# Optimization experiments

Hardware: AMD Instinct MI355X
Metric: run time of the kernel (lower is better)

Reference implementation:

```python
import jax, jax.numpy as jnp
import numpy as np

B, S, LW = 128, 256, 20          # batch, sent len, max word len
VW, VC = 400000, 80              # word / char vocab
DC, DW, HC, HW, NT = 25, 300, 25, 200, 10  # dims from args.dims; NT tags
DIN = DW + 2 * HC                # word-LSTM input dim = 350


def setup_inputs() -> dict:
    key = jax.random.key(0)
    ks = jax.random.split(key, 16)
    s = 0.1
    return {
        "words_batch": jax.random.randint(ks[0], (B, S), 0, VW),
        "chars_batch": jax.random.randint(ks[1], (B, S, LW), 0, VC),
        "lens_word": jnp.sort(jax.random.randint(ks[2], (B,), 1, S + 1))[::-1],
        "emb_char": jax.random.normal(ks[3], (VC + 1, DC), jnp.float32) * s,
        "emb_word": jax.random.normal(ks[4], (VW, DW), jnp.float32) * s,
        "conv_w": jax.random.normal(ks[5], (2 * HC, 1, 3, DC), jnp.float32) * s,
        "conv_b": jnp.zeros((2 * HC,), jnp.float32),
        "w_ih_f": jax.random.normal(ks[6], (4 * HW, DIN), jnp.float32) * s,
        "w_hh_f": jax.random.normal(ks[7], (4 * HW, HW), jnp.float32) * s,
        "b_f": jnp.zeros((4 * HW,), jnp.float32),
        "w_ih_b": jax.random.normal(ks[8], (4 * HW, DIN), jnp.float32) * s,
        "w_hh_b": jax.random.normal(ks[9], (4 * HW, HW), jnp.float32) * s,
        "b_b": jnp.zeros((4 * HW,), jnp.float32),
        "proj_w": jax.random.normal(ks[10], (NT, 2 * HW), jnp.float32) * s,
        "proj_b": jnp.zeros((NT,), jnp.float32),
    }


def _lstm_dir(xg, w_hh, mask, reverse):
    # xg: [S,B,4H] precomputed input-gate contributions; mask: [S,B,1]
    Hh = w_hh.shape[1]
    h0 = jnp.zeros((xg.shape[1], Hh), xg.dtype)
    c0 = jnp.zeros_like(h0)

    def step(carry, inp):
        h, c = carry
        xg_t, m = inp
        g = xg_t + h @ w_hh.T
        i, f, gg, o = jnp.split(g, 4, axis=-1)
        i, f, o = jax.nn.sigmoid(i), jax.nn.sigmoid(f), jax.nn.sigmoid(o)
        gg = jnp.tanh(gg)
        c_new = f * c + i * gg
        h_new = o * jnp.tanh(c_new)
        h = jnp.where(m, h_new, h)
        c = jnp.where(m, c_new, c)
        out = jnp.where(m, h_new, 0.0)  # pad_packed zeros beyond length
        return (h, c), out

    _, out = jax.lax.scan(step, (h0, c0), (xg, mask), reverse=reverse)
    return out  # [S,B,H]


def reference(words_batch, chars_batch, lens_word, emb_char, emb_word,
              conv_w, conv_b, w_ih_f, w_hh_f, b_f, w_ih_b, w_hh_b, b_b,
              proj_w, proj_b):
    # --- char CNN encoder ---
    ec = emb_char[chars_batch]                       # [B,S,LW,DC]
    x = ec.reshape(B * S, 1, LW, DC)
    y = jax.lax.conv_general_dilated(x, conv_w, (1, 1), [(2, 2), (0, 0)])
    y = y + conv_b[None, :, None, None]              # [B*S, 2HC, LW+2, 1]
    out_char = y.max(axis=(2, 3)).reshape(B, S, 2 * HC)
    # --- word features ---
    ew = emb_word[words_batch]                       # [B,S,DW]
    feats = jnp.concatenate([ew, out_char], axis=-1) # [B,S,DIN]
    # --- masked BiLSTM over words (packed-sequence semantics) ---
    mask = (jnp.arange(S)[None, :] < lens_word[:, None])  # [B,S]
    mask_t = mask.T[:, :, None]                      # [S,B,1]
    xf = jnp.einsum('bsd,gd->sbg', feats, w_ih_f) + b_f
    xb = jnp.einsum('bsd,gd->sbg', feats, w_ih_b) + b_b
    hf = _lstm_dir(xf, w_hh_f, mask_t, reverse=False)
    hb = _lstm_dir(xb, w_hh_b, mask_t, reverse=True)
    enc = jnp.concatenate([hf, hb], axis=-1).transpose(1, 0, 2)  # [B,S,2HW]
    # --- emissions ---
    return jnp.einsum('bsh,th->bst', enc, proj_w) + proj_b       # [B,S,NT]
```

## Files before the change

kernel.cpp:

```cpp
#include <hip/hip_runtime.h>

typedef unsigned short u16;
typedef __attribute__((ext_vector_type(4))) unsigned short u16x4;
typedef __attribute__((ext_vector_type(8))) short bf16x8;
typedef __attribute__((ext_vector_type(4))) float f32x4;

#define BB 128
#define SS 256
#define LWW 20
#define NTg 10
#define HWg 200
#define G4 800
#define DWg 300
#define DIN 350
#define KP 352
#define NP 896
#define NW (BB*SS)
#define OUTN (NW*NTg)

__device__ __forceinline__ float b2f(u16 u){ return __uint_as_float(((unsigned)u)<<16); }
__device__ __forceinline__ u16 f2b(float f){
  unsigned x = __float_as_uint(f);
  unsigned r = (x + 0x7fffu + ((x>>16)&1u)) >> 16;
  return (u16)r;
}
__device__ __forceinline__ float ldf(const void* p, long long i, int isb){
  return isb ? b2f(((const u16*)p)[i]) : ((const float*)p)[i];
}
__device__ __forceinline__ int ldi(const void* p, long long i, int i64){
  return i64 ? (int)((const long long*)p)[i] : ((const int*)p)[i];
}
__device__ __forceinline__ f32x4 mfma16(bf16x8 a, bf16x8 b, f32x4 c){
  return __builtin_amdgcn_mfma_f32_16x16x32_bf16(a,b,c,0,0,0);
}
__device__ __forceinline__ float sigf(float x){
  return __builtin_amdgcn_rcpf(1.f + __expf(-x));
}
__device__ __forceinline__ float tanhf_(float x){
  return 1.f - 2.f*__builtin_amdgcn_rcpf(1.f + __expf(2.f*x));
}

__global__ void k_diag(float* out, float code){
  int i = blockIdx.x*256 + threadIdx.x;
  if(i<OUTN) out[i]=code;
}

__global__ void k_probe(const void* p, int* flag){
  __shared__ int cnt;
  if(threadIdx.x==0) cnt=0;
  __syncthreads();
  float a = fabsf(b2f(((const u16*)p)[threadIdx.x]));
  if(a>1e-5f && a<1.0f) atomicAdd(&cnt,1);
  __syncthreads();
  if(threadIdx.x==0) *flag = (cnt>=100)?1:0;
}
__global__ void k_probe_int(const int* __restrict__ words, int* iflag){
  __shared__ int zc;
  if(threadIdx.x==0) zc=0;
  __syncthreads();
  int z=0;
  for(int k=threadIdx.x;k<128;k+=64)
    if(words[2*k+1]==0) z++;
  atomicAdd(&zc,z);
  __syncthreads();
  if(threadIdx.x==0) *iflag = (zc>=100)?1:0;
}

__global__ void k_stage_wih(const void* __restrict__ src, u16* __restrict__ dst,
                            const int* __restrict__ flag){
  int isb=*flag;
  int i = blockIdx.x*256 + threadIdx.x;
  if(i>=NP*KP) return;
  int n=i/KP, k=i-n*KP;
  float v = (n<G4 && k<DIN) ? ldf(src,(long long)n*DIN+k,isb) : 0.f;
  dst[i]=f2b(v);
}
__global__ void k_stage_whh(const void* __restrict__ src, u16* __restrict__ dst,
                            const int* __restrict__ flag){
  int isb=*flag;
  int i = blockIdx.x*256 + threadIdx.x;
  if(i>=179200) return;
  int tile=i/3584, r=i%3584, ks=r/512, r2=r%512, l=r2/8, jreg=r2%8;
  int c = tile*16 + (l&15);
  int j = c>>2, gate = c&3;
  int n = gate*200 + j;
  int k = ks*32 + ((l>>4)<<3) + jreg;
  float v = (k<HWg)? ldf(src,(long long)n*HWg+k,isb) : 0.f;
  dst[i]=f2b(v);
}
__global__ void k_stage_misc(const void* echar, const void* convw, const void* cb,
                             const void* bfp, const void* bbp, const void* pw, const void* pb,
                             float* d_ec, float* d_cw, float* d_cb,
                             float* d_bf, float* d_bb, float* d_pw, float* d_pb,
                             const int* __restrict__ flag){
  int isb=*flag;
  int i = blockIdx.x*256 + threadIdx.x;
  if(i<2025){ d_ec[i]=ldf(echar,i,isb); return; } i-=2025;
  if(i<3750){ d_cw[i]=ldf(convw,i,isb); return; } i-=3750;
  if(i<64){ d_cb[i]=(i<50)?ldf(cb,i,isb):0.f; return; } i-=64;
  if(i<800){ d_bf[i]=ldf(bfp,i,isb); return; } i-=800;
  if(i<800){ d_bb[i]=ldf(bbp,i,isb); return; } i-=800;
  if(i<4000){ d_pw[i]=ldf(pw,i,isb); return; } i-=4000;
  if(i<16){ d_pb[i]=(i<10)?ldf(pb,i,isb):0.f; return; }
}

__global__ void k_gather(const void* __restrict__ words, const void* __restrict__ embw,
                         u16* __restrict__ feats,
                         const int* __restrict__ flag, const int* __restrict__ iflag){
  int isb=*flag, i64=*iflag;
  int wv=threadIdx.x>>6, lane=threadIdx.x&63;
  int row = blockIdx.x*4 + wv;
  int idx = ldi(words,row,i64);
  u16* d = feats + (size_t)row*KP;
  if(isb){
    const u16* s=(const u16*)embw + (long long)idx*DWg;
    for(int c=lane;c<DWg;c+=64) d[c]=s[c];
  } else {
    const float* s=(const float*)embw + (long long)idx*DWg;
    for(int c=lane;c<DWg;c+=64) d[c]=f2b(s[c]);
  }
  if(lane<2) d[350+lane]=0;
}

__global__ __launch_bounds__(256) void k_char(const void* __restrict__ chars,
                      const float* __restrict__ ec, const float* __restrict__ cw,
                      const float* __restrict__ cb, u16* __restrict__ feats,
                      const int* __restrict__ iflag){
  int i64=*iflag;
  int gid = blockIdx.x*256 + threadIdx.x;
  int w = gid/50, f = gid - w*50;
  int ch[20];
  #pragma unroll
  for(int r=0;r<20;r++) ch[r]=ldi(chars,(long long)w*LWW+r,i64);
  float acc[22];
  #pragma unroll
  for(int t=0;t<22;t++) acc[t]=0.f;
  for(int c=0;c<25;c++){
    float wv0=cw[(f*3+0)*25+c];
    float wv1=cw[(f*3+1)*25+c];
    float wv2=cw[(f*3+2)*25+c];
    #pragma unroll
    for(int r=0;r<20;r++){
      float xv = ec[ch[r]*25+c];
      acc[r+2] += xv*wv0;
      acc[r+1] += xv*wv1;
      acc[r]   += xv*wv2;
    }
  }
  float m=-1e30f;
  #pragma unroll
  for(int t=0;t<22;t++) m=fmaxf(m,acc[t]);
  feats[(size_t)w*KP + 300 + f] = f2b(m + cb[f]);
}

__global__ __launch_bounds__(256) void k_gemm(const u16* __restrict__ feats,
                      const u16* __restrict__ wih, const float* __restrict__ bias,
                      u16* __restrict__ xg){
  __shared__ u16 At[128*40];
  __shared__ u16 Bt[128*40];
  int tid=threadIdx.x, m0=blockIdx.x*128, n0=blockIdx.y*128;
  int wv=tid>>6, lane=tid&63;
  int wr=(wv>>1)*64, wc=(wv&1)*64;
  const f32x4 z4={0.f,0.f,0.f,0.f};
  f32x4 acc[4][4];
  #pragma unroll
  for(int a=0;a<4;a++){ acc[a][0]=z4; acc[a][1]=z4; acc[a][2]=z4; acc[a][3]=z4; }
  int row=tid>>2, grp=tid&3;
  for(int kt=0;kt<11;kt++){
    int k0=kt*32;
    #pragma unroll
    for(int p=0;p<2;p++){
      int r=row+p*64;
      *(int4*)&At[r*40+grp*8] = *(const int4*)&feats[(size_t)(m0+r)*KP + k0 + grp*8];
      *(int4*)&Bt[r*40+grp*8] = *(const int4*)&wih  [(size_t)(n0+r)*KP + k0 + grp*8];
    }
    __syncthreads();
    bf16x8 af[4], bg[4];
    #pragma unroll
    for(int ri=0;ri<4;ri++) af[ri]=*(const bf16x8*)&At[(wr+ri*16+(lane&15))*40 + ((lane>>4)<<3)];
    #pragma unroll
    for(int ni=0;ni<4;ni++) bg[ni]=*(const bf16x8*)&Bt[(wc+ni*16+(lane&15))*40 + ((lane>>4)<<3)];
    #pragma unroll
    for(int ri=0;ri<4;ri++)
      #pragma unroll
      for(int ni=0;ni<4;ni++) acc[ri][ni]=mfma16(af[ri],bg[ni],acc[ri][ni]);
    __syncthreads();
  }
  #pragma unroll
  for(int ni=0;ni<4;ni++){
    int n = n0 + wc + ni*16 + (lane&15);
    if(n>=G4) continue;
    float bv = bias[n];
    int g4=n/200, j=n-g4*200;
    #pragma unroll
    for(int ri=0;ri<4;ri++)
      #pragma unroll
      for(int rr=0;rr<4;rr++){
        int m = m0 + wr + ri*16 + ((lane>>4)&3)*4 + rr;
        int b = m>>8, s = m&255;
        xg[((size_t)s*BB + b)*G4 + j*4 + g4] = f2b(acc[ri][ni][rr] + bv);
      }
  }
}

__global__ __launch_bounds__(512,1) void k_lstm(
    const u16* __restrict__ xgf, const u16* __restrict__ xgb,
    const u16* __restrict__ whhf, const u16* __restrict__ whhb,
    const void* __restrict__ lens, u16* __restrict__ enc,
    const int* __restrict__ iflag)
{
  __shared__ u16 hbuf[2][16*232];
  __shared__ int len_s[16];
  __shared__ u16 wlds[7168];

  const int blk=blockIdx.x, dir=blk&1, b0=(blk>>1)*16;
  const u16* xg  = dir? xgb : xgf;
  const u16* whh = dir? whhb : whhf;
  const int tid=threadIdx.x, wv=tid>>6, lane=tid&63;
  const int i64=*iflag;

  for(int i=tid;i<2*16*232;i+=512) ((u16*)hbuf)[i]=0;
  if(tid<16) len_s[tid]=ldi(lens,b0+tid,i64);
  for(int i=tid;i<7168;i+=512) wlds[i]=whh[48*3584 + i];

  bf16x8 wf[6][7];
  #pragma unroll
  for(int i=0;i<6;i++)
    #pragma unroll
    for(int ks=0;ks<7;ks++)
      wf[i][ks]=*(const bf16x8*)&whh[(size_t)((wv*6+i)*7+ks)*512 + lane*8];

  const int bl = lane&15;
  const int jq = lane>>4;
  __syncthreads();
  const int lenv = len_s[bl];

  int xoff[7], eoff[7], hboff[7];
  #pragma unroll
  for(int q=0;q<6;q++){
    int j=(wv*6+q)*4+jq;
    xoff[q]=(b0+bl)*G4 + j*4;
    eoff[q]=((b0+bl)*SS)*(2*HWg) + dir*HWg + j;
    hboff[q]=bl*232 + j;
  }
  { int j=(48+wv)*4+jq;
    xoff[6]=(b0+bl)*G4 + j*4;
    eoff[6]=((b0+bl)*SS)*(2*HWg) + dir*HWg + j;
    hboff[6]=bl*232 + j; }

  float cst[7]={0,0,0,0,0,0,0}, hreg[7]={0,0,0,0,0,0,0};

  const int t0 = dir? (SS-1):0;
  const int dstep = dir? -1:1;
  const u16* xg_t = xg + (size_t)t0*(BB*G4);
  u16* enc_t = enc + (size_t)t0*(2*HWg);

  u16x4 xr[7];
  #pragma unroll
  for(int q=0;q<6;q++) xr[q]=*(const u16x4*)&xg_t[xoff[q]];
  if(wv<2) xr[6]=*(const u16x4*)&xg_t[xoff[6]];

  const f32x4 z4={0.f,0.f,0.f,0.f};
  int cur=0;
  for(int step=0; step<SS; ++step){
    const int t = dir ? (SS-1-step) : step;
    const u16* hc = hbuf[cur];
    u16* hn_ = hbuf[cur^1];
    const u16* xg_n = (step<SS-1)? (xg_t + dstep*(BB*G4)) : xg_t;

    bf16x8 afr[7];
    #pragma unroll
    for(int ks=0;ks<7;ks++)
      afr[ks]=*(const bf16x8*)&hc[(lane&15)*232 + ks*32 + ((lane>>4)<<3)];

    f32x4 acc[7];
    #pragma unroll
    for(int i=0;i<6;i++){
      acc[i]=z4;
      #pragma unroll
      for(int ks=0;ks<7;ks++) acc[i]=mfma16(wf[i][ks],afr[ks],acc[i]);
    }
    acc[6]=z4;
    if(wv<2){
      #pragma unroll
      for(int ks=0;ks<7;ks++){
        bf16x8 bw=*(const bf16x8*)&wlds[(wv*7+ks)*512 + lane*8];
        acc[6]=mfma16(bw,afr[ks],acc[6]);
      }
    }

    const bool msk = t < lenv;
    #pragma unroll
    for(int q=0;q<7;q++){
      if(q==6 && wv>=2) break;
      float gi=acc[q][0]+b2f(xr[q].x);
      float gf=acc[q][1]+b2f(xr[q].y);
      float gg=acc[q][2]+b2f(xr[q].z);
      float go=acc[q][3]+b2f(xr[q].w);
      float iv=sigf(gi), fv=sigf(gf), gv=tanhf_(gg), ov=sigf(go);
      float cn=fv*cst[q]+iv*gv;
      float hv=ov*tanhf_(cn);
      if(msk){ cst[q]=cn; hreg[q]=hv; }
      enc_t[eoff[q]] = msk? f2b(hv):(u16)0;
      hn_[hboff[q]] = f2b(hreg[q]);
      xr[q]=*(const u16x4*)&xg_n[xoff[q]];
    }

    xg_t = xg_n;
    enc_t += dstep*(2*HWg);
    __syncthreads();
    cur^=1;
  }
}

__global__ __launch_bounds__(256) void k_emis(const u16* __restrict__ enc,
                      const float* __restrict__ pw_g, const float* __restrict__ pb,
                      float* __restrict__ out){
  __shared__ float pw[10*404];
  int tid=threadIdx.x;
  for(int i=tid;i<4000;i+=256){ int tg=i/400,h=i-tg*400; pw[tg*404+h]=pw_g[i]; }
  __syncthreads();
  int idx = blockIdx.x*256 + tid;
  int bs = idx/NTg, tg = idx-bs*NTg;
  const u16* er = enc + (size_t)bs*(2*HWg);
  float acc=0.f;
  #pragma unroll 4
  for(int h=0;h<400;h+=4){
    u16x4 v=*(const u16x4*)&er[h];
    acc += b2f(v.x)*pw[tg*404+h]   + b2f(v.y)*pw[tg*404+h+1]
         + b2f(v.z)*pw[tg*404+h+2] + b2f(v.w)*pw[tg*404+h+3];
  }
  out[idx] = acc + pb[tg];
}

extern "C" void kernel_launch(void* const* d_in, const int* in_sizes, int n_in,
                              void* d_out, int out_size, void* d_ws, size_t ws_size,
                              hipStream_t stream){
  float* out=(float*)d_out;
  if(n_in!=15){ k_diag<<<1280,256,0,stream>>>(out, 20480.f); return; }
  if(out_size!=OUTN){ k_diag<<<1280,256,0,stream>>>(out, 24576.f); return; }

  const void* words=d_in[0];
  const void* chars=d_in[1];
  const void* lens =d_in[2];
  const void* echar=d_in[3];
  const void* embw =d_in[4];
  const void* convw=d_in[5];
  const void* convb=d_in[6];
  const void* wihf =d_in[7];
  const void* whhf =d_in[8];
  const void* bfp  =d_in[9];
  const void* wihb =d_in[10];
  const void* whhb =d_in[11];
  const void* bbp  =d_in[12];
  const void* pw   =d_in[13];
  const void* pb   =d_in[14];

  char* ws=(char*)d_ws;
  size_t cur=0;
  auto alloc=[&](size_t sz){ size_t o=cur; cur=(cur+sz+255)&~(size_t)255; return o; };
  size_t oF    = alloc(4);
  size_t oIF   = alloc(4);
  size_t oWIHF = alloc((size_t)NP*KP*2);
  size_t oWIHB = alloc((size_t)NP*KP*2);
  size_t oWHHF = alloc(179200*2);
  size_t oWHHB = alloc(179200*2);
  size_t oEC   = alloc(2025*4);
  size_t oCW   = alloc(3750*4);
  size_t oCB   = alloc(64*4);
  size_t oBF   = alloc(800*4);
  size_t oBB   = alloc(800*4);
  size_t oPW   = alloc(4000*4);
  size_t oPB   = alloc(16*4);
  size_t oSH   = alloc((size_t)NW*2*HWg*2);
  size_t oXGF  = alloc((size_t)SS*BB*G4*2);
  size_t oXGB  = alloc((size_t)SS*BB*G4*2);
  size_t need  = cur;

  if(ws_size < need){
    k_diag<<<1280,256,0,stream>>>(out, 16384.f + 64.f*(float)(ws_size>>20));
    return;
  }

  int*   flag =(int*)(ws+oF);
  int*   iflag=(int*)(ws+oIF);
  u16*   sWIHF=(u16*)(ws+oWIHF);
  u16*   sWIHB=(u16*)(ws+oWIHB);
  u16*   sWHHF=(u16*)(ws+oWHHF);
  u16*   sWHHB=(u16*)(ws+oWHHB);
  float* sEC  =(float*)(ws+oEC);
  float* sCW  =(float*)(ws+oCW);
  float* sCB  =(float*)(ws+oCB);
  float* sBF  =(float*)(ws+oBF);
  float* sBB  =(float*)(ws+oBB);
  float* sPW  =(float*)(ws+oPW);
  float* sPB  =(float*)(ws+oPB);
  u16*   feats=(u16*)(ws+oSH);
  u16*   enc  =(u16*)(ws+oSH);
  u16*   xgfp =(u16*)(ws+oXGF);
  u16*   xgbp =(u16*)(ws+oXGB);

  k_probe<<<1,128,0,stream>>>(embw, flag);
  k_probe_int<<<1,64,0,stream>>>((const int*)words, iflag);
  k_stage_wih<<<1232,256,0,stream>>>(wihf, sWIHF, flag);
  k_stage_wih<<<1232,256,0,stream>>>(wihb, sWIHB, flag);
  k_stage_whh<<<700,256,0,stream>>>(whhf, sWHHF, flag);
  k_stage_whh<<<700,256,0,stream>>>(whhb, sWHHB, flag);
  k_stage_misc<<<45,256,0,stream>>>(echar, convw, convb, bfp, bbp, pw, pb,
                                    sEC, sCW, sCB, sBF, sBB, sPW, sPB, flag);
  k_gather<<<8192,256,0,stream>>>(words, embw, feats, flag, iflag);
  k_char<<<6400,256,0,stream>>>(chars, sEC, sCW, sCB, feats, iflag);
  k_gemm<<<dim3(256,7),256,0,stream>>>(feats, sWIHF, sBF, xgfp);
  k_gemm<<<dim3(256,7),256,0,stream>>>(feats, sWIHB, sBB, xgbp);
  k_lstm<<<16,512,0,stream>>>(xgfp, xgbp, sWHHF, sWHHB, lens, enc, iflag);
  k_emis<<<1280,256,0,stream>>>(enc, sPW, sPB, out);
}
```

Baseline: 1.663 ms.

## Stage LSTM gate inputs through LDS and write hidden states coalesced

The recurrent LSTM kernel now prefetches each next timestep's 16-sequence gate-input slab with coalesced 16-byte loads into a double-buffered LDS array. Each thread then reads its gate values from LDS instead of doing scattered 8-byte global loads. Hidden outputs are written one step late, straight from the shared h buffer, as contiguous per-block slabs in new separate forward/backward enc layouts, and the emission kernel is adapted to read them. This is meant to cut global-memory latency on the serial 256-step critical path, at the cost of about 80KB of dynamic LDS and extra LDS traffic per step.

```diff
diff --git a/kernel.cpp b/kernel.cpp
--- a/kernel.cpp
+++ b/kernel.cpp
@@ -206,20 +206,23 @@
 __global__ __launch_bounds__(512,1) void k_lstm(
     const u16* __restrict__ xgf, const u16* __restrict__ xgb,
     const u16* __restrict__ whhf, const u16* __restrict__ whhb,
-    const void* __restrict__ lens, u16* __restrict__ enc,
+    const void* __restrict__ lens, u16* __restrict__ encf, u16* __restrict__ encb,
     const int* __restrict__ iflag)
 {
-  __shared__ u16 hbuf[2][16*232];
-  __shared__ int len_s[16];
-  __shared__ u16 wlds[7168];
+  extern __shared__ char smem[];
+  u16* xbuf = (u16*)smem;
+  u16* hbuf = (u16*)(smem + 51712);
+  u16* wlds = (u16*)(smem + 51712 + 14848);
+  int* len_s = (int*)(smem + 51712 + 14848 + 14336);
 
   const int blk=blockIdx.x, dir=blk&1, b0=(blk>>1)*16;
   const u16* xg  = dir? xgb : xgf;
   const u16* whh = dir? whhb : whhf;
+  u16* encd = (dir? encb : encf) + (size_t)(blk>>1)*SS*3200;
   const int tid=threadIdx.x, wv=tid>>6, lane=tid&63;
   const int i64=*iflag;
 
-  for(int i=tid;i<2*16*232;i+=512) ((u16*)hbuf)[i]=0;
+  for(int i=tid;i<16*232;i+=512) hbuf[i]=0;
   if(tid<16) len_s[tid]=ldi(lens,b0+tid,i64);
   for(int i=tid;i<7168;i+=512) wlds[i]=whh[48*3584 + i];
 
@@ -232,47 +235,60 @@
 
   const int bl = lane&15;
   const int jq = lane>>4;
-  __syncthreads();
-  const int lenv = len_s[bl];
-
-  int xoff[7], eoff[7], hboff[7];
+
+  int xoff[7], hboff[7];
   #pragma unroll
   for(int q=0;q<6;q++){
     int j=(wv*6+q)*4+jq;
-    xoff[q]=(b0+bl)*G4 + j*4;
-    eoff[q]=((b0+bl)*SS)*(2*HWg) + dir*HWg + j;
+    xoff[q]=bl*808 + j*4;
     hboff[q]=bl*232 + j;
   }
-  { int j=(48+wv)*4+jq;
-    xoff[6]=(b0+bl)*G4 + j*4;
-    eoff[6]=((b0+bl)*SS)*(2*HWg) + dir*HWg + j;
-    hboff[6]=bl*232 + j; }
-
-  float cst[7]={0,0,0,0,0,0,0}, hreg[7]={0,0,0,0,0,0,0};
+  { int j=(48+wv)*4+jq; xoff[6]=bl*808 + j*4; hboff[6]=bl*232 + j; }
 
   const int t0 = dir? (SS-1):0;
   const int dstep = dir? -1:1;
-  const u16* xg_t = xg + (size_t)t0*(BB*G4);
-  u16* enc_t = enc + (size_t)t0*(2*HWg);
-
-  u16x4 xr[7];
-  #pragma unroll
-  for(int q=0;q<6;q++) xr[q]=*(const u16x4*)&xg_t[xoff[q]];
-  if(wv<2) xr[6]=*(const u16x4*)&xg_t[xoff[6]];
+
+  {
+    const u16* src = xg + (size_t)(t0*BB + b0)*G4;
+    #pragma unroll
+    for(int k=0;k<4;k++){
+      int i2 = tid + k*512;
+      if(i2<1600){
+        int4 v = *(const int4*)&src[i2*8];
+        int blc = i2/100, d = i2-blc*100;
+        *(int4*)&xbuf[blc*808 + d*8] = v;
+      }
+    }
+  }
+  float cst[7]={0,0,0,0,0,0,0}, hreg[7]={0,0,0,0,0,0,0};
+  __syncthreads();
+  const int lenv = len_s[bl];
 
   const f32x4 z4={0.f,0.f,0.f,0.f};
   int cur=0;
   for(int step=0; step<SS; ++step){
     const int t = dir ? (SS-1-step) : step;
-    const u16* hc = hbuf[cur];
-    u16* hn_ = hbuf[cur^1];
-    const u16* xg_n = (step<SS-1)? (xg_t + dstep*(BB*G4)) : xg_t;
+    int sn = step+1; if(sn>SS-1) sn=SS-1;
+    const int tn = dir ? (SS-1-sn) : sn;
+
+    int4 xgr0,xgr1,xgr2,xgr3;
+    {
+      const u16* src = xg + (size_t)(tn*BB + b0)*G4;
+      xgr0 = *(const int4*)&src[(size_t)tid*8];
+      xgr1 = *(const int4*)&src[(size_t)(tid+512)*8];
+      xgr2 = *(const int4*)&src[(size_t)(tid+1024)*8];
+      xgr3 = (tid<64)? *(const int4*)&src[(size_t)(tid+1536)*8] : xgr0;
+    }
+
+    const u16* hc = hbuf + cur*(16*232);
+    u16* hn_ = hbuf + (cur^1)*(16*232);
+    const u16* xc = xbuf + cur*(16*808);
+    u16* xn_ = xbuf + (cur^1)*(16*808);
 
     bf16x8 afr[7];
     #pragma unroll
     for(int ks=0;ks<7;ks++)
       afr[ks]=*(const bf16x8*)&hc[(lane&15)*232 + ks*32 + ((lane>>4)<<3)];
-
     f32x4 acc[7];
     #pragma unroll
     for(int i=0;i<6;i++){
@@ -289,31 +305,70 @@
       }
     }
 
+    if(step>0){
+      const int tp = t - dstep;
+      u16* dst = encd + (size_t)tp*3200;
+      #pragma unroll
+      for(int k=0;k<4;k++){
+        int i2 = tid + k*512;
+        if(i2<1600){
+          int blc = i2/100, d = i2-blc*100;
+          unsigned v = *(const unsigned*)&hc[blc*232 + d*2];
+          if(tp >= len_s[blc]) v = 0u;
+          *(unsigned*)&dst[i2*2] = v;
+        }
+      }
+    }
+
+    #pragma unroll
+    for(int k=0;k<4;k++){
+      int i2 = tid + k*512;
+      if(i2<1600){
+        int blc = i2/100, d = i2-blc*100;
+        int4 v = (k==0)? xgr0 : (k==1)? xgr1 : (k==2)? xgr2 : xgr3;
+        *(int4*)&xn_[blc*808 + d*8] = v;
+      }
+    }
+
     const bool msk = t < lenv;
     #pragma unroll
     for(int q=0;q<7;q++){
       if(q==6 && wv>=2) break;
-      float gi=acc[q][0]+b2f(xr[q].x);
-      float gf=acc[q][1]+b2f(xr[q].y);
-      float gg=acc[q][2]+b2f(xr[q].z);
-      float go=acc[q][3]+b2f(xr[q].w);
+      u16x4 xrv = *(const u16x4*)&xc[xoff[q]];
+      float gi=acc[q][0]+b2f(xrv.x);
+      float gf=acc[q][1]+b2f(xrv.y);
+      float gg=acc[q][2]+b2f(xrv.z);
+      float go=acc[q][3]+b2f(xrv.w);
       float iv=sigf(gi), fv=sigf(gf), gv=tanhf_(gg), ov=sigf(go);
       float cn=fv*cst[q]+iv*gv;
       float hv=ov*tanhf_(cn);
       if(msk){ cst[q]=cn; hreg[q]=hv; }
-      enc_t[eoff[q]] = msk? f2b(hv):(u16)0;
       hn_[hboff[q]] = f2b(hreg[q]);
-      xr[q]=*(const u16x4*)&xg_n[xoff[q]];
-    }
-
-    xg_t = xg_n;
-    enc_t += dstep*(2*HWg);
+    }
+
     __syncthreads();
     cur^=1;
   }
-}
-
-__global__ __launch_bounds__(256) void k_emis(const u16* __restrict__ enc,
+
+  {
+    const int tl = dir? 0 : SS-1;
+    const u16* hc = hbuf + cur*(16*232);
+    u16* dst = encd + (size_t)tl*3200;
+    #pragma unroll
+    for(int k=0;k<4;k++){
+      int i2 = tid + k*512;
+      if(i2<1600){
+        int blc = i2/100, d = i2-blc*100;
+        unsigned v = *(const unsigned*)&hc[blc*232 + d*2];
+        if(tl >= len_s[blc]) v = 0u;
+        *(unsigned*)&dst[i2*2] = v;
+      }
+    }
+  }
+}
+
+__global__ __launch_bounds__(256) void k_emis(const u16* __restrict__ encf,
+                      const u16* __restrict__ encb,
                       const float* __restrict__ pw_g, const float* __restrict__ pb,
                       float* __restrict__ out){
   __shared__ float pw[10*404];
@@ -322,13 +377,22 @@
   __syncthreads();
   int idx = blockIdx.x*256 + tid;
   int bs = idx/NTg, tg = idx-bs*NTg;
-  const u16* er = enc + (size_t)bs*(2*HWg);
+  int b = bs>>8, s = bs&255;
+  size_t base = ((size_t)(b>>4)*SS + s)*3200 + (size_t)(b&15)*200;
+  const u16* erf = encf + base;
+  const u16* erb = encb + base;
   float acc=0.f;
   #pragma unroll 4
-  for(int h=0;h<400;h+=4){
-    u16x4 v=*(const u16x4*)&er[h];
+  for(int h=0;h<200;h+=4){
+    u16x4 v=*(const u16x4*)&erf[h];
     acc += b2f(v.x)*pw[tg*404+h]   + b2f(v.y)*pw[tg*404+h+1]
          + b2f(v.z)*pw[tg*404+h+2] + b2f(v.w)*pw[tg*404+h+3];
+  }
+  #pragma unroll 4
+  for(int h=0;h<200;h+=4){
+    u16x4 v=*(const u16x4*)&erb[h];
+    acc += b2f(v.x)*pw[tg*404+200+h]   + b2f(v.y)*pw[tg*404+200+h+1]
+         + b2f(v.z)*pw[tg*404+200+h+2] + b2f(v.w)*pw[tg*404+200+h+3];
   }
   out[idx] = acc + pb[tg];
 }
@@ -396,7 +460,8 @@
   float* sPW  =(float*)(ws+oPW);
   float* sPB  =(float*)(ws+oPB);
   u16*   feats=(u16*)(ws+oSH);
-  u16*   enc  =(u16*)(ws+oSH);
+  u16*   encf =(u16*)(ws+oSH);
+  u16*   encb =(u16*)(ws+oSH + (size_t)NW*HWg*2);
   u16*   xgfp =(u16*)(ws+oXGF);
   u16*   xgbp =(u16*)(ws+oXGB);
 
@@ -412,6 +477,6 @@
   k_char<<<6400,256,0,stream>>>(chars, sEC, sCW, sCB, feats, iflag);
   k_gemm<<<dim3(256,7),256,0,stream>>>(feats, sWIHF, sBF, xgfp);
   k_gemm<<<dim3(256,7),256,0,stream>>>(feats, sWIHB, sBB, xgbp);
-  k_lstm<<<16,512,0,stream>>>(xgfp, xgbp, sWHHF, sWHHB, lens, enc, iflag);
-  k_emis<<<1280,256,0,stream>>>(enc, sPW, sPB, out);
-}
+  k_lstm<<<16,512,80960,stream>>>(xgfp, xgbp, sWHHF, sWHHB, lens, encf, encb, iflag);
+  k_emis<<<1280,256,0,stream>>>(encf, encb, sPW, sPB, out);
+}
```

Measured after the change: 1.680 ms. No clear change (+1.1%).
